# Kernel optimization log

Measured on AMD Instinct MI355X. Metric: run time of the kernel, lower is better.

The kernel has to match this reference:

```python
import jax, jax.numpy as jnp
import numpy as np

B, P, S, D, H, DFF, VOC = 8, 16, 512, 512, 8, 2048, 10000
DEPTH = D // H
SIGMA = 0.1
T = 256
LN_EPS = 1e-6


def setup_inputs() -> dict:
    key = jax.random.key(0)
    ks = jax.random.split(key, 40)
    n = lambda i, sh, sc=1.0: jax.random.normal(ks[i], sh, jnp.float32) * sc
    inp = {
        "r": n(0, (B, P, D)),
        "x": jax.random.randint(ks[1], (B, 1), 0, VOC),
        "K": n(2, (B, P, S, D)),
        "Vs": n(3, (B, P, S, D)),
        "w": jax.random.uniform(ks[4], (B, P, 1), jnp.float32),
        "I": jax.random.randint(ks[5], (B, P, S), 0, P),
        "t": T,
        "eps_q": n(6, (B, P, 1, D)),
        "eps_k": n(7, (B, P, 1, D)),
        "eps_v": n(8, (B, P, 1, D)),
        "eps_z": n(9, (B, P, 1, D)),
        "gumbel": -jnp.log(-jnp.log(jax.random.uniform(ks[10], (B, P, P), jnp.float32, 1e-8, 1.0))),
        "Wq": n(11, (D, D), 0.02), "bq": jnp.zeros((D,), jnp.float32),
        "Wk": n(12, (D, D), 0.02), "bk": jnp.zeros((D,), jnp.float32),
        "Wv": n(13, (D, D), 0.02), "bv": jnp.zeros((D,), jnp.float32),
        "Wo": n(14, (D, D), 0.02), "bo": jnp.zeros((D,), jnp.float32),
        "ln1_g": jnp.ones((D,), jnp.float32), "ln1_b": jnp.zeros((D,), jnp.float32),
        "ln3_g": jnp.ones((D,), jnp.float32), "ln3_b": jnp.zeros((D,), jnp.float32),
        "W1": n(15, (D, DFF), 0.02), "b1": jnp.zeros((DFF,), jnp.float32),
        "W2": n(16, (DFF, D), 0.02), "b2": jnp.zeros((D,), jnp.float32),
        "Wout": n(17, (D, VOC), 0.02), "bout": jnp.zeros((VOC,), jnp.float32),
    }
    return inp


def _layernorm(x, g, b):
    mu = jnp.mean(x, axis=-1, keepdims=True)
    var = jnp.mean((x - mu) ** 2, axis=-1, keepdims=True)
    return (x - mu) / jnp.sqrt(var + LN_EPS) * g + b


def _split_heads(x):  # (B,P,L,D) -> (B,P,H,L,depth)
    b, p, l, _ = x.shape
    return x.reshape(b, p, l, H, DEPTH).transpose(0, 1, 3, 2, 4)


def _resample(params, i_t, t):  # reorder particle axis on prefix [:t+1]
    pref = jnp.take_along_axis(params[:, :, :t + 1], i_t[:, :, None, None], axis=1)
    return jnp.concatenate([pref, params[:, :, t + 1:]], axis=2)


def reference(r, x, K, Vs, w, I, t, eps_q, eps_k, eps_v, eps_z, gumbel,
              Wq, bq, Wk, bk, Wv, bv, Wo, bo, ln1_g, ln1_b, ln3_g, ln3_b,
              W1, b1, W2, b2, Wout, bout):
    x = x.astype(jnp.int32)
    I = I.astype(jnp.int32)
    r4 = r[:, :, None, :]                                   # (B,P,1,D)
    # --- mha_smc: noisy projections + K/V buffer update at t ---
    q = r4 @ Wq + bq + SIGMA * eps_q
    k = r4 @ Wk + bk + SIGMA * eps_k
    v = r4 @ Wv + bv + SIGMA * eps_v
    K = K.at[:, :, t, :].set(k[:, :, 0, :])
    Vs = Vs.at[:, :, t, :].set(v[:, :, 0, :])
    qh = _split_heads(q)                                    # (B,P,H,1,depth)
    Kh = _split_heads(K)                                    # (B,P,H,S,depth)
    Vh = _split_heads(Vs)
    scores = jnp.einsum('bphqd,bphsd->bphqs', qh, Kh) / jnp.sqrt(jnp.float32(DEPTH))
    mask = (jnp.arange(S) <= t)[None, None, None, None, :]
    scores = jnp.where(mask, scores, jnp.float32(-1e9))
    attn = jax.nn.softmax(scores, axis=-1)                  # (B,P,H,1,S)
    zh = jnp.einsum('bphqs,bphsd->bphqd', attn, Vh)
    z = zh.transpose(0, 1, 3, 2, 4).reshape(B, P, 1, D) @ Wo + bo
    z = z + SIGMA * eps_z                                   # reparametrized output noise
    attn_weights = jnp.mean(attn, axis=2)                   # (B,P,1,S)
    # --- residual + FFN (dropout disabled: training=False) ---
    out1 = _layernorm(z + r4, ln1_g, ln1_b)
    ffn = jnp.maximum(out1 @ W1 + b1, 0.0) @ W2 + b2
    r_ = _layernorm(ffn + out1, ln3_g, ln3_b)
    predictions = r_ @ Wout + bout                          # (B,P,1,VOC)
    # --- classification importance weights ---
    probs = jax.nn.softmax(predictions, axis=-1)
    idx = jnp.broadcast_to(x.reshape(B, 1, 1, 1), (B, P, 1, 1))
    w_sq = jnp.take_along_axis(probs, idx, axis=-1)[:, :, 0, 0]  # (B,P)
    w_sq = jax.lax.stop_gradient(w_sq)
    pred2 = predictions[:, :, 0, :]                         # (B,P,VOC)
    w_for_pred = w_sq[:, :, None]
    good_avg_pred = jnp.mean(pred2, axis=1, keepdims=True)  # (B,1,VOC)
    avg_pred_after_softmax = jnp.mean(jax.nn.softmax(pred2, axis=-1), axis=1, keepdims=True)
    argmax_w = jnp.argmax(w_for_pred, axis=1)               # (B,1)
    max_prediction = jnp.take_along_axis(pred2, argmax_w[:, :, None], axis=1)  # (B,1,VOC)
    # --- sample_and_keep_indices: Gumbel-max categorical over particles ---
    logits = jnp.log(w_sq + 1e-10)                          # (B,P)
    i_t = jnp.argmax(logits[:, None, :] + gumbel, axis=-1).astype(jnp.int32)  # (B,P)
    I_pref = jnp.take_along_axis(I[:, :, :t], i_t[:, :, None], axis=1)
    I_new = jnp.concatenate([I_pref, i_t[:, :, None], I[:, :, t + 1:]], axis=2)
    # --- resampling (faithful to original: V resampled from already-resampled K) ---
    K = _resample(K, i_t, t)
    Vs = _resample(K, i_t, t)
    z = jnp.take_along_axis(z, I_new[:, :, t][:, :, None, None], axis=1)
    w_new = w_sq[:, :, None]
    return (r4, z, avg_pred_after_softmax, good_avg_pred, max_prediction,
            eps_z, attn_weights, K, Vs, w_new, I_new)
```

## Files before the change

### kernel.cpp

```cpp
#include <hip/hip_runtime.h>

#define NDFF 2048
#define NVOC 10000
#define SIGMA 0.1f

typedef float f32x4 __attribute__((ext_vector_type(4)));

#define O0 0
#define O1 65536
#define O2 131072
#define O3 211072
#define O4 291072
#define O5 371072
#define O6 436608
#define O7 502144
#define O8 34056576
#define O9 67611008
#define O10 67611136

#define WQ    0
#define WK    65536
#define WV    131072
#define WZH   196608
#define WZ    262144
#define WO1   327680
#define WH1   393216
#define WR    655360
#define WPRED 720896
#define WMAX  2000896
#define WSUM  2001024
#define WWSQ  2001152
#define WIT   2001280
#define WF2P  2001536
#define WSC   2263680

__global__ __launch_bounds__(512)
void k_qkv(const float* __restrict__ r,
           const float* __restrict__ Wq, const float* __restrict__ bq, const float* __restrict__ eq, float* __restrict__ oq,
           const float* __restrict__ Wk, const float* __restrict__ bk, const float* __restrict__ ek, float* __restrict__ ok,
           const float* __restrict__ Wv, const float* __restrict__ bv, const float* __restrict__ ev, float* __restrict__ ov)
{
    const float *W, *bias, *eps; float* out;
    if (blockIdx.z == 0)      { W = Wq; bias = bq; eps = eq; out = oq; }
    else if (blockIdx.z == 1) { W = Wk; bias = bk; eps = ek; out = ok; }
    else                      { W = Wv; bias = bv; eps = ev; out = ov; }
    int tid = threadIdx.x;
    int col = tid & 63, kq = tid >> 6;
    int colg = blockIdx.x * 64 + col;
    int row0 = blockIdx.y * 8;
    __shared__ float rs[8][512];
#pragma unroll
    for (int j = 0; j < 8; j++) {
        int idx = tid + j * 512;
        rs[idx >> 9][idx & 511] = r[(row0 + (idx >> 9)) * 512 + (idx & 511)];
    }
    __syncthreads();
    float acc[8] = {0,0,0,0,0,0,0,0};
    const float* Wp = W + (kq * 64) * 512 + colg;
#pragma unroll 8
    for (int d = 0; d < 64; d++) {
        float wv = Wp[d * 512];
#pragma unroll
        for (int p = 0; p < 8; p++) acc[p] += rs[p][kq * 64 + d] * wv;
    }
    __syncthreads();
    float (*part)[8][64] = (float(*)[8][64])rs;
#pragma unroll
    for (int p = 0; p < 8; p++) part[kq][p][col] = acc[p];
    __syncthreads();
    {
        int p = tid >> 6, c = tid & 63;
        int cg = blockIdx.x * 64 + c;
        float v = 0.f;
#pragma unroll
        for (int k = 0; k < 8; k++) v += part[k][p][c];
        out[(row0 + p) * 512 + cg] = v + bias[cg] + SIGMA * eps[(row0 + p) * 512 + cg];
    }
}

__global__ __launch_bounds__(256)
void k_attn(const float* __restrict__ qws, const float* __restrict__ kws,
            const float* __restrict__ vws, const float* __restrict__ Kin,
            const float* __restrict__ Vin, const int* __restrict__ t_ptr,
            float* __restrict__ zh, float* __restrict__ scw)
{
    int t = *t_ptr;
    int bp = blockIdx.x, h = blockIdx.y;
    int tid = threadIdx.x;
    int wave = tid >> 6, lane = tid & 63;
    __shared__ float sc[512];
    __shared__ float red[4], red2[4];
    __shared__ float part[4][64];

    float4 qv = ((const float4*)(qws + bp * 512 + h * 64))[lane & 15];

    for (int sb = wave * 4; sb <= t; sb += 16) {
        int s = sb + (lane >> 4);
        bool valid = (s <= t);
        int ss = valid ? s : t;
        const float4* kr = (ss == t) ? (const float4*)(kws + bp * 512 + h * 64)
                                     : (const float4*)(Kin + (bp * 512 + ss) * 512 + h * 64);
        float4 kv = kr[lane & 15];
        float p = qv.x * kv.x + qv.y * kv.y + qv.z * kv.z + qv.w * kv.w;
#pragma unroll
        for (int m = 1; m < 16; m <<= 1) p += __shfl_xor(p, m, 64);
        if ((lane & 15) == 0 && valid) sc[s] = p * 0.125f;
    }
    __syncthreads();

    float lm = -3.0e38f;
    for (int s = tid; s <= t; s += 256) lm = fmaxf(lm, sc[s]);
#pragma unroll
    for (int o = 32; o; o >>= 1) lm = fmaxf(lm, __shfl_xor(lm, o, 64));
    if (lane == 0) red[wave] = lm;
    __syncthreads();
    float m = fmaxf(fmaxf(red[0], red[1]), fmaxf(red[2], red[3]));
    float ls = 0.f;
    for (int s = tid; s <= t; s += 256) ls += __expf(sc[s] - m);
#pragma unroll
    for (int o = 32; o; o >>= 1) ls += __shfl_xor(ls, o, 64);
    if (lane == 0) red2[wave] = ls;
    __syncthreads();
    float inv = 1.f / (red2[0] + red2[1] + red2[2] + red2[3]);
    for (int s = tid; s <= t; s += 256) {
        float a = __expf(sc[s] - m) * inv;
        sc[s] = a;
        scw[(bp * 8 + h) * 512 + s] = a;
    }
    __syncthreads();

    float acc = 0.f;
    const float* Vp = Vin + (bp * 512) * 512 + h * 64 + lane;
    int s = wave;
    for (; s + 12 < t; s += 16) {
        float v0 = __builtin_nontemporal_load(Vp + (size_t)(s     ) * 512);
        float v1 = __builtin_nontemporal_load(Vp + (size_t)(s +  4) * 512);
        float v2 = __builtin_nontemporal_load(Vp + (size_t)(s +  8) * 512);
        float v3 = __builtin_nontemporal_load(Vp + (size_t)(s + 12) * 512);
        acc += sc[s] * v0 + sc[s + 4] * v1 + sc[s + 8] * v2 + sc[s + 12] * v3;
    }
    for (; s < t; s += 4) acc += sc[s] * __builtin_nontemporal_load(Vp + (size_t)s * 512);
    if ((t & 3) == wave) acc += sc[t] * vws[bp * 512 + h * 64 + lane];
    part[wave][lane] = acc;
    __syncthreads();
    if (tid < 64)
        zh[bp * 512 + h * 64 + tid] = part[0][tid] + part[1][tid] + part[2][tid] + part[3][tid];
}

__global__ __launch_bounds__(512)
void k_zproj(const float* __restrict__ zh, const float* __restrict__ Wo,
             const float* __restrict__ bo, const float* __restrict__ epsz,
             float* __restrict__ out)
{
    int tid = threadIdx.x;
    int col = tid & 63, kq = tid >> 6;
    int colg = blockIdx.x * 64 + col;
    int row0 = blockIdx.y * 8;
    __shared__ float rs[8][512];
#pragma unroll
    for (int j = 0; j < 8; j++) {
        int idx = tid + j * 512;
        rs[idx >> 9][idx & 511] = zh[(row0 + (idx >> 9)) * 512 + (idx & 511)];
    }
    __syncthreads();
    float acc[8] = {0,0,0,0,0,0,0,0};
    const float* Wp = Wo + (kq * 64) * 512 + colg;
#pragma unroll 8
    for (int d = 0; d < 64; d++) {
        float wv = Wp[d * 512];
#pragma unroll
        for (int p = 0; p < 8; p++) acc[p] += rs[p][kq * 64 + d] * wv;
    }
    __syncthreads();
    float (*part)[8][64] = (float(*)[8][64])rs;
#pragma unroll
    for (int p = 0; p < 8; p++) part[kq][p][col] = acc[p];
    __syncthreads();
    {
        int p = tid >> 6, c = tid & 63;
        int cg = blockIdx.x * 64 + c;
        float v = 0.f;
#pragma unroll
        for (int k = 0; k < 8; k++) v += part[k][p][c];
        out[(row0 + p) * 512 + cg] = v + bo[cg] + SIGMA * epsz[(row0 + p) * 512 + cg];
    }
}

__global__ __launch_bounds__(512)
void k_ln(const float* __restrict__ a, const float* __restrict__ b,
          const float* __restrict__ g, const float* __restrict__ beta,
          float* __restrict__ out)
{
    __shared__ float red[8];
    int row = blockIdx.x, tid = threadIdx.x;
    float x = a[row * 512 + tid] + b[row * 512 + tid];
    float s = x;
#pragma unroll
    for (int o = 32; o; o >>= 1) s += __shfl_xor(s, o, 64);
    if ((tid & 63) == 0) red[tid >> 6] = s;
    __syncthreads();
    float tot = 0.f;
#pragma unroll
    for (int i = 0; i < 8; i++) tot += red[i];
    float mu = tot * (1.f / 512.f);
    float dx = x - mu;
    float s2 = dx * dx;
#pragma unroll
    for (int o = 32; o; o >>= 1) s2 += __shfl_xor(s2, o, 64);
    __syncthreads();
    if ((tid & 63) == 0) red[tid >> 6] = s2;
    __syncthreads();
    float tot2 = 0.f;
#pragma unroll
    for (int i = 0; i < 8; i++) tot2 += red[i];
    float var = tot2 * (1.f / 512.f);
    out[row * 512 + tid] = dx * rsqrtf(var + 1e-6f) * g[tid] + beta[tid];
}

__global__ __launch_bounds__(512)
void k_ln_sum4(const float* __restrict__ f2p, const float* __restrict__ b2,
               const float* __restrict__ o1, const float* __restrict__ g,
               const float* __restrict__ beta, float* __restrict__ out)
{
    __shared__ float red[8];
    int row = blockIdx.x, tid = threadIdx.x;
    int idx = row * 512 + tid;
    float x = f2p[idx] + f2p[65536 + idx] + f2p[131072 + idx] + f2p[196608 + idx]
            + b2[tid] + o1[idx];
    float s = x;
#pragma unroll
    for (int o = 32; o; o >>= 1) s += __shfl_xor(s, o, 64);
    if ((tid & 63) == 0) red[tid >> 6] = s;
    __syncthreads();
    float tot = 0.f;
#pragma unroll
    for (int i = 0; i < 8; i++) tot += red[i];
    float mu = tot * (1.f / 512.f);
    float dx = x - mu;
    float s2 = dx * dx;
#pragma unroll
    for (int o = 32; o; o >>= 1) s2 += __shfl_xor(s2, o, 64);
    __syncthreads();
    if ((tid & 63) == 0) red[tid >> 6] = s2;
    __syncthreads();
    float tot2 = 0.f;
#pragma unroll
    for (int i = 0; i < 8; i++) tot2 += red[i];
    float var = tot2 * (1.f / 512.f);
    out[idx] = dx * rsqrtf(var + 1e-6f) * g[tid] + beta[tid];
}

__global__ __launch_bounds__(512)
void k_ffn1(const float* __restrict__ in, const float* __restrict__ W1,
            const float* __restrict__ b1, float* __restrict__ h1)
{
    int tid = threadIdx.x;
    int col = tid & 63, kq = tid >> 6;
    int colg = blockIdx.x * 64 + col;
    int row0 = blockIdx.y * 8;
    __shared__ float rs[8][512];
#pragma unroll
    for (int j = 0; j < 8; j++) {
        int idx = tid + j * 512;
        rs[idx >> 9][idx & 511] = in[(row0 + (idx >> 9)) * 512 + (idx & 511)];
    }
    __syncthreads();
    float acc[8] = {0,0,0,0,0,0,0,0};
    const float* Wp = W1 + (kq * 64) * NDFF + colg;
#pragma unroll 8
    for (int d = 0; d < 64; d++) {
        float wv = Wp[d * NDFF];
#pragma unroll
        for (int p = 0; p < 8; p++) acc[p] += rs[p][kq * 64 + d] * wv;
    }
    __syncthreads();
    float (*part)[8][64] = (float(*)[8][64])rs;
#pragma unroll
    for (int p = 0; p < 8; p++) part[kq][p][col] = acc[p];
    __syncthreads();
    {
        int p = tid >> 6, c = tid & 63;
        int cg = blockIdx.x * 64 + c;
        float v = 0.f;
#pragma unroll
        for (int k = 0; k < 8; k++) v += part[k][p][c];
        h1[(row0 + p) * NDFF + cg] = fmaxf(v + b1[cg], 0.f);
    }
}

__global__ __launch_bounds__(512)
void k_ffn2p(const float* __restrict__ h1, const float* __restrict__ W2,
             float* __restrict__ f2p)
{
    int tid = threadIdx.x;
    int col = tid & 63, kq = tid >> 6;
    int colg = blockIdx.x * 64 + col;
    int row0 = blockIdx.y * 8;
    int ks = blockIdx.z;
    __shared__ float rs[8][512];
#pragma unroll
    for (int j = 0; j < 8; j++) {
        int idx = tid + j * 512;
        rs[idx >> 9][idx & 511] = h1[(row0 + (idx >> 9)) * NDFF + ks * 512 + (idx & 511)];
    }
    __syncthreads();
    float acc[8] = {0,0,0,0,0,0,0,0};
    const float* Wp = W2 + (ks * 512 + kq * 64) * 512 + colg;
#pragma unroll 8
    for (int d = 0; d < 64; d++) {
        float wv = Wp[d * 512];
#pragma unroll
        for (int p = 0; p < 8; p++) acc[p] += rs[p][kq * 64 + d] * wv;
    }
    __syncthreads();
    float (*part)[8][64] = (float(*)[8][64])rs;
#pragma unroll
    for (int p = 0; p < 8; p++) part[kq][p][col] = acc[p];
    __syncthreads();
    {
        int p = tid >> 6, c = tid & 63;
        int cg = blockIdx.x * 64 + c;
        float v = 0.f;
#pragma unroll
        for (int k = 0; k < 8; k++) v += part[k][p][c];
        f2p[ks * 65536 + (row0 + p) * 512 + cg] = v;
    }
}

__global__ __launch_bounds__(512)
void k_pred(const float* __restrict__ r_, const float* __restrict__ Wout,
            const float* __restrict__ bout, float* __restrict__ pred)
{
    int tid = threadIdx.x;
    int col = tid & 255, kh = tid >> 8;
    int colg = blockIdx.x * 256 + col;
    int colL = min(colg, NVOC - 1);
    int row0 = blockIdx.y * 16;
    __shared__ float rs[16][512];
#pragma unroll
    for (int j = 0; j < 16; j++) {
        int idx = tid + j * 512;
        rs[idx >> 9][idx & 511] = r_[(row0 + (idx >> 9)) * 512 + (idx & 511)];
    }
    __syncthreads();
    float acc[16];
#pragma unroll
    for (int p = 0; p < 16; p++) acc[p] = 0.f;
    const float* Wp = Wout + (kh * 256) * NVOC + colL;
#pragma unroll 4
    for (int d = 0; d < 256; d++) {
        float wv = Wp[d * NVOC];
#pragma unroll
        for (int p = 0; p < 16; p++) acc[p] += rs[p][kh * 256 + d] * wv;
    }
    __syncthreads();
    float (*part)[256] = (float(*)[256])rs;
    if (kh == 1) {
#pragma unroll
        for (int p = 0; p < 16; p++) part[p][col] = acc[p];
    }
    __syncthreads();
    if (kh == 0 && colg < NVOC) {
        float bv = bout[colg];
#pragma unroll
        for (int p = 0; p < 16; p++)
            pred[(row0 + p) * NVOC + colg] = acc[p] + part[p][col] + bv;
    }
}

__global__ __launch_bounds__(512)
void k_soft(const float* __restrict__ pred, const int* __restrict__ x,
            const float* __restrict__ scw, const int* __restrict__ t_ptr,
            float* __restrict__ rowmax, float* __restrict__ rowsum,
            float* __restrict__ wsq, float* __restrict__ out)
{
    __shared__ float red[8];
    int row = blockIdx.x, tid = threadIdx.x;
    {
        int t = *t_ptr;
        float a = 0.f;
        if (tid <= t) {
#pragma unroll
            for (int hh = 0; hh < 8; hh++) a += scw[(row * 8 + hh) * 512 + tid];
            a *= 0.125f;
        }
        out[O6 + row * 512 + tid] = a;
    }
    const float* pr = pred + row * NVOC;
    float m = -3.0e38f;
    for (int v = tid; v < NVOC; v += 512) m = fmaxf(m, pr[v]);
#pragma unroll
    for (int o = 32; o; o >>= 1) m = fmaxf(m, __shfl_xor(m, o, 64));
    if ((tid & 63) == 0) red[tid >> 6] = m;
    __syncthreads();
#pragma unroll
    for (int i = 0; i < 8; i++) m = fmaxf(m, red[i]);
    __syncthreads();
    float s = 0.f;
    for (int v = tid; v < NVOC; v += 512) s += __expf(pr[v] - m);
#pragma unroll
    for (int o = 32; o; o >>= 1) s += __shfl_xor(s, o, 64);
    if ((tid & 63) == 0) red[tid >> 6] = s;
    __syncthreads();
    if (tid == 0) {
        float tot = 0.f;
#pragma unroll
        for (int i = 0; i < 8; i++) tot += red[i];
        rowmax[row] = m; rowsum[row] = tot;
        int b = row >> 4;
        float w = __expf(pr[x[b]] - m) / tot;
        wsq[row] = w;
        out[O9 + row] = w;
    }
}

__global__ __launch_bounds__(512)
void k_vocab(const float* __restrict__ pred, const float* __restrict__ rowmax,
             const float* __restrict__ rowsum, const float* __restrict__ wsq,
             const float* __restrict__ gumbel, int* __restrict__ it,
             float* __restrict__ out)
{
    int b = blockIdx.y;
    int tid = threadIdx.x;
    __shared__ int s_amw;
    if (tid == 0) {
        float bw = -3.0e38f; int bj = 0;
#pragma unroll
        for (int pp = 0; pp < 16; pp++) {
            float wv = wsq[b * 16 + pp];
            if (wv > bw) { bw = wv; bj = pp; }
        }
        s_amw = bj;
    }
    if (blockIdx.x == 0 && tid < 16) {
        float best = -3.0e38f; int bi = 0;
#pragma unroll
        for (int pp = 0; pp < 16; pp++) {
            float v = logf(wsq[b * 16 + pp] + 1e-10f) + gumbel[(b * 16 + tid) * 16 + pp];
            if (v > best) { best = v; bi = pp; }
        }
        it[b * 16 + tid] = bi;
    }
    __syncthreads();
    int v = blockIdx.x * 512 + tid;
    if (v >= NVOC) return;
    int amw = s_amw;
    float ga = 0.f, as = 0.f;
#pragma unroll
    for (int p = 0; p < 16; p++) {
        int rr = b * 16 + p;
        float pv = pred[rr * NVOC + v];
        ga += pv;
        as += __expf(pv - rowmax[rr]) * (1.f / rowsum[rr]);
    }
    out[O3 + b * NVOC + v] = ga * (1.f / 16.f);
    out[O2 + b * NVOC + v] = as * (1.f / 16.f);
    out[O4 + b * NVOC + v] = pred[(b * 16 + amw) * NVOC + v];
}

__global__ __launch_bounds__(256)
void k_resample(const float* __restrict__ Kin, const float* __restrict__ kws,
                const int* __restrict__ it, const int* __restrict__ t_ptr,
                const float* __restrict__ r, const float* __restrict__ epsz,
                const float* __restrict__ zws, const int* __restrict__ Iin,
                float* __restrict__ out)
{
    int t = *t_ptr;
    const f32x4* K4  = (const f32x4*)Kin;
    const f32x4* kw4 = (const f32x4*)kws;
    const f32x4* r4  = (const f32x4*)r;
    const f32x4* e4  = (const f32x4*)epsz;
    const f32x4* z4  = (const f32x4*)zws;
    f32x4* oK = (f32x4*)(out + O7);
    f32x4* oV = (f32x4*)(out + O8);
    const int total = 128 * 512 * 128;
    const int total2 = total + 16384;
    for (int i = blockIdx.x * 256 + threadIdx.x; i < total2; i += gridDim.x * 256) {
        if (i < total) {
            int lane = i & 127;
            int row = i >> 7;
            int s = row & 511;
            int bp = row >> 9;
            int b = bp >> 4;
            f32x4 vK, vV;
            if (s > t) {
                vK = __builtin_nontemporal_load(&K4[i]);
                vV = vK;
            } else {
                int ip = it[bp];
                int ip2 = it[b * 16 + ip];
                if (s == t) {
                    vK = kw4[(b * 16 + ip) * 128 + lane];
                    vV = kw4[(b * 16 + ip2) * 128 + lane];
                } else {
                    vK = K4[((b * 16 + ip) * 512 + s) * 128 + lane];
                    vV = K4[((b * 16 + ip2) * 512 + s) * 128 + lane];
                }
            }
            __builtin_nontemporal_store(vK, &oK[i]);
            __builtin_nontemporal_store(vV, &oV[i]);
        } else {
            int j = i - total;
            int fidx = j * 4;
            ((f32x4*)(out + O0))[j] = r4[j];
            ((f32x4*)(out + O5))[j] = e4[j];
            int row = fidx >> 9, d0 = fidx & 511;
            int b = row >> 4;
            int ip = it[row];
            ((f32x4*)(out + O1))[j] = z4[((b * 16 + ip) << 7) + (d0 >> 2)];
#pragma unroll
            for (int k = 0; k < 4; k++) {
                int s = d0 + k;
                float iv;
                if (s < t)       iv = (float)Iin[((b * 16 + ip) << 9) + s];
                else if (s == t) iv = (float)ip;
                else             iv = (float)Iin[row * 512 + s];
                out[O10 + fidx + k] = iv;
            }
        }
    }
}

extern "C" void kernel_launch(void* const* d_in, const int* in_sizes, int n_in,
                              void* d_out, int out_size, void* d_ws, size_t ws_size,
                              hipStream_t stream) {
    const float* r      = (const float*)d_in[0];
    const int*   x      = (const int*)d_in[1];
    const float* Kin    = (const float*)d_in[2];
    const float* Vin    = (const float*)d_in[3];
    const int*   Iin    = (const int*)d_in[5];
    const int*   t_ptr  = (const int*)d_in[6];
    const float* eps_q  = (const float*)d_in[7];
    const float* eps_k  = (const float*)d_in[8];
    const float* eps_v  = (const float*)d_in[9];
    const float* eps_z  = (const float*)d_in[10];
    const float* gumbel = (const float*)d_in[11];
    const float* Wq = (const float*)d_in[12]; const float* bq = (const float*)d_in[13];
    const float* Wk = (const float*)d_in[14]; const float* bk = (const float*)d_in[15];
    const float* Wv = (const float*)d_in[16]; const float* bv = (const float*)d_in[17];
    const float* Wo = (const float*)d_in[18]; const float* bo = (const float*)d_in[19];
    const float* ln1_g = (const float*)d_in[20]; const float* ln1_b = (const float*)d_in[21];
    const float* ln3_g = (const float*)d_in[22]; const float* ln3_b = (const float*)d_in[23];
    const float* W1 = (const float*)d_in[24]; const float* b1 = (const float*)d_in[25];
    const float* W2 = (const float*)d_in[26]; const float* b2 = (const float*)d_in[27];
    const float* Wout = (const float*)d_in[28]; const float* bout = (const float*)d_in[29];

    float* ws  = (float*)d_ws;
    float* q   = ws + WQ;
    float* kv  = ws + WK;
    float* vv  = ws + WV;
    float* zh  = ws + WZH;
    float* zp  = ws + WZ;
    float* o1  = ws + WO1;
    float* h1  = ws + WH1;
    float* rr  = ws + WR;
    float* pr  = ws + WPRED;
    float* rmx = ws + WMAX;
    float* rsm = ws + WSUM;
    float* wsq = ws + WWSQ;
    int*   itw = (int*)(ws + WIT);
    float* f2p = ws + WF2P;
    float* scw = ws + WSC;
    float* outp = (float*)d_out;

    k_qkv<<<dim3(8, 16, 3), 512, 0, stream>>>(r, Wq, bq, eps_q, q, Wk, bk, eps_k, kv, Wv, bv, eps_v, vv);
    k_attn<<<dim3(128, 8), 256, 0, stream>>>(q, kv, vv, Kin, Vin, t_ptr, zh, scw);
    k_zproj<<<dim3(8, 16), 512, 0, stream>>>(zh, Wo, bo, eps_z, zp);
    k_ln<<<128, 512, 0, stream>>>(zp, r, ln1_g, ln1_b, o1);
    k_ffn1<<<dim3(32, 16), 512, 0, stream>>>(o1, W1, b1, h1);
    k_ffn2p<<<dim3(8, 16, 4), 512, 0, stream>>>(h1, W2, f2p);
    k_ln_sum4<<<128, 512, 0, stream>>>(f2p, b2, o1, ln3_g, ln3_b, rr);
    k_pred<<<dim3(40, 8), 512, 0, stream>>>(rr, Wout, bout, pr);
    k_soft<<<128, 512, 0, stream>>>(pr, x, scw, t_ptr, rmx, rsm, wsq, outp);
    k_vocab<<<dim3(20, 8), 512, 0, stream>>>(pr, rmx, rsm, wsq, gumbel, itw, outp);
    k_resample<<<4096, 256, 0, stream>>>(Kin, kv, itw, t_ptr, r, eps_z, zp, Iin, outp);
}
```

Before: 199.8 us.

## Fuse layernorms into FFN1 and prediction GEMMs, widen attention blocks

The two standalone layernorm kernels are removed. LN1 is recomputed inside each k_ffn1 block, with the x==0 blocks writing o1. LN3, together with the four-way f2p split-K sum, moves into k_pred's shared-memory prologue. This drops two launches and the intermediate round trip through global memory, at the cost of redundant layernorm work in every column block. Attention blocks also grow from 256 to 512 threads so each block streams more V rows in parallel.

```diff
diff --git a/kernel.cpp b/kernel.cpp
--- a/kernel.cpp
+++ b/kernel.cpp
@@ -25,7 +25,6 @@
 #define WZ    262144
 #define WO1   327680
 #define WH1   393216
-#define WR    655360
 #define WPRED 720896
 #define WMAX  2000896
 #define WSUM  2001024
@@ -50,10 +49,7 @@
     int row0 = blockIdx.y * 8;
     __shared__ float rs[8][512];
 #pragma unroll
-    for (int j = 0; j < 8; j++) {
-        int idx = tid + j * 512;
-        rs[idx >> 9][idx & 511] = r[(row0 + (idx >> 9)) * 512 + (idx & 511)];
-    }
+    for (int j = 0; j < 8; j++) rs[j][tid & 511] = r[(row0 + j) * 512 + tid];
     __syncthreads();
     float acc[8] = {0,0,0,0,0,0,0,0};
     const float* Wp = W + (kq * 64) * 512 + colg;
@@ -78,7 +74,7 @@
     }
 }
 
-__global__ __launch_bounds__(256)
+__global__ __launch_bounds__(512)
 void k_attn(const float* __restrict__ qws, const float* __restrict__ kws,
             const float* __restrict__ vws, const float* __restrict__ Kin,
             const float* __restrict__ Vin, const int* __restrict__ t_ptr,
@@ -89,12 +85,12 @@
     int tid = threadIdx.x;
     int wave = tid >> 6, lane = tid & 63;
     __shared__ float sc[512];
-    __shared__ float red[4], red2[4];
-    __shared__ float part[4][64];
+    __shared__ float red[8], red2[8];
+    __shared__ float part[8][64];
 
     float4 qv = ((const float4*)(qws + bp * 512 + h * 64))[lane & 15];
 
-    for (int sb = wave * 4; sb <= t; sb += 16) {
+    for (int sb = wave * 4; sb <= t; sb += 32) {
         int s = sb + (lane >> 4);
         bool valid = (s <= t);
         int ss = valid ? s : t;
@@ -109,20 +105,25 @@
     __syncthreads();
 
     float lm = -3.0e38f;
-    for (int s = tid; s <= t; s += 256) lm = fmaxf(lm, sc[s]);
+    for (int s = tid; s <= t; s += 512) lm = fmaxf(lm, sc[s]);
 #pragma unroll
     for (int o = 32; o; o >>= 1) lm = fmaxf(lm, __shfl_xor(lm, o, 64));
     if (lane == 0) red[wave] = lm;
     __syncthreads();
-    float m = fmaxf(fmaxf(red[0], red[1]), fmaxf(red[2], red[3]));
+    float m = red[0];
+#pragma unroll
+    for (int i = 1; i < 8; i++) m = fmaxf(m, red[i]);
     float ls = 0.f;
-    for (int s = tid; s <= t; s += 256) ls += __expf(sc[s] - m);
+    for (int s = tid; s <= t; s += 512) ls += __expf(sc[s] - m);
 #pragma unroll
     for (int o = 32; o; o >>= 1) ls += __shfl_xor(ls, o, 64);
     if (lane == 0) red2[wave] = ls;
     __syncthreads();
-    float inv = 1.f / (red2[0] + red2[1] + red2[2] + red2[3]);
-    for (int s = tid; s <= t; s += 256) {
+    float tot = 0.f;
+#pragma unroll
+    for (int i = 0; i < 8; i++) tot += red2[i];
+    float inv = 1.f / tot;
+    for (int s = tid; s <= t; s += 512) {
         float a = __expf(sc[s] - m) * inv;
         sc[s] = a;
         scw[(bp * 8 + h) * 512 + s] = a;
@@ -132,19 +133,23 @@
     float acc = 0.f;
     const float* Vp = Vin + (bp * 512) * 512 + h * 64 + lane;
     int s = wave;
-    for (; s + 12 < t; s += 16) {
+    for (; s + 24 < t; s += 32) {
         float v0 = __builtin_nontemporal_load(Vp + (size_t)(s     ) * 512);
-        float v1 = __builtin_nontemporal_load(Vp + (size_t)(s +  4) * 512);
-        float v2 = __builtin_nontemporal_load(Vp + (size_t)(s +  8) * 512);
-        float v3 = __builtin_nontemporal_load(Vp + (size_t)(s + 12) * 512);
-        acc += sc[s] * v0 + sc[s + 4] * v1 + sc[s + 8] * v2 + sc[s + 12] * v3;
-    }
-    for (; s < t; s += 4) acc += sc[s] * __builtin_nontemporal_load(Vp + (size_t)s * 512);
-    if ((t & 3) == wave) acc += sc[t] * vws[bp * 512 + h * 64 + lane];
+        float v1 = __builtin_nontemporal_load(Vp + (size_t)(s +  8) * 512);
+        float v2 = __builtin_nontemporal_load(Vp + (size_t)(s + 16) * 512);
+        float v3 = __builtin_nontemporal_load(Vp + (size_t)(s + 24) * 512);
+        acc += sc[s] * v0 + sc[s + 8] * v1 + sc[s + 16] * v2 + sc[s + 24] * v3;
+    }
+    for (; s < t; s += 8) acc += sc[s] * __builtin_nontemporal_load(Vp + (size_t)s * 512);
+    if ((t & 7) == wave) acc += sc[t] * vws[bp * 512 + h * 64 + lane];
     part[wave][lane] = acc;
     __syncthreads();
-    if (tid < 64)
-        zh[bp * 512 + h * 64 + tid] = part[0][tid] + part[1][tid] + part[2][tid] + part[3][tid];
+    if (tid < 64) {
+        float v = 0.f;
+#pragma unroll
+        for (int k = 0; k < 8; k++) v += part[k][tid];
+        zh[bp * 512 + h * 64 + tid] = v;
+    }
 }
 
 __global__ __launch_bounds__(512)
@@ -158,10 +163,7 @@
     int row0 = blockIdx.y * 8;
     __shared__ float rs[8][512];
 #pragma unroll
-    for (int j = 0; j < 8; j++) {
-        int idx = tid + j * 512;
-        rs[idx >> 9][idx & 511] = zh[(row0 + (idx >> 9)) * 512 + (idx & 511)];
-    }
+    for (int j = 0; j < 8; j++) rs[j][tid] = zh[(row0 + j) * 512 + tid];
     __syncthreads();
     float acc[8] = {0,0,0,0,0,0,0,0};
     const float* Wp = Wo + (kq * 64) * 512 + colg;
@@ -187,82 +189,42 @@
 }
 
 __global__ __launch_bounds__(512)
-void k_ln(const float* __restrict__ a, const float* __restrict__ b,
-          const float* __restrict__ g, const float* __restrict__ beta,
-          float* __restrict__ out)
-{
-    __shared__ float red[8];
-    int row = blockIdx.x, tid = threadIdx.x;
-    float x = a[row * 512 + tid] + b[row * 512 + tid];
-    float s = x;
-#pragma unroll
-    for (int o = 32; o; o >>= 1) s += __shfl_xor(s, o, 64);
-    if ((tid & 63) == 0) red[tid >> 6] = s;
-    __syncthreads();
-    float tot = 0.f;
-#pragma unroll
-    for (int i = 0; i < 8; i++) tot += red[i];
-    float mu = tot * (1.f / 512.f);
-    float dx = x - mu;
-    float s2 = dx * dx;
-#pragma unroll
-    for (int o = 32; o; o >>= 1) s2 += __shfl_xor(s2, o, 64);
-    __syncthreads();
-    if ((tid & 63) == 0) red[tid >> 6] = s2;
-    __syncthreads();
-    float tot2 = 0.f;
-#pragma unroll
-    for (int i = 0; i < 8; i++) tot2 += red[i];
-    float var = tot2 * (1.f / 512.f);
-    out[row * 512 + tid] = dx * rsqrtf(var + 1e-6f) * g[tid] + beta[tid];
-}
-
-__global__ __launch_bounds__(512)
-void k_ln_sum4(const float* __restrict__ f2p, const float* __restrict__ b2,
-               const float* __restrict__ o1, const float* __restrict__ g,
-               const float* __restrict__ beta, float* __restrict__ out)
-{
-    __shared__ float red[8];
-    int row = blockIdx.x, tid = threadIdx.x;
-    int idx = row * 512 + tid;
-    float x = f2p[idx] + f2p[65536 + idx] + f2p[131072 + idx] + f2p[196608 + idx]
-            + b2[tid] + o1[idx];
-    float s = x;
-#pragma unroll
-    for (int o = 32; o; o >>= 1) s += __shfl_xor(s, o, 64);
-    if ((tid & 63) == 0) red[tid >> 6] = s;
-    __syncthreads();
-    float tot = 0.f;
-#pragma unroll
-    for (int i = 0; i < 8; i++) tot += red[i];
-    float mu = tot * (1.f / 512.f);
-    float dx = x - mu;
-    float s2 = dx * dx;
-#pragma unroll
-    for (int o = 32; o; o >>= 1) s2 += __shfl_xor(s2, o, 64);
-    __syncthreads();
-    if ((tid & 63) == 0) red[tid >> 6] = s2;
-    __syncthreads();
-    float tot2 = 0.f;
-#pragma unroll
-    for (int i = 0; i < 8; i++) tot2 += red[i];
-    float var = tot2 * (1.f / 512.f);
-    out[idx] = dx * rsqrtf(var + 1e-6f) * g[tid] + beta[tid];
-}
-
-__global__ __launch_bounds__(512)
-void k_ffn1(const float* __restrict__ in, const float* __restrict__ W1,
-            const float* __restrict__ b1, float* __restrict__ h1)
+void k_ffn1(const float* __restrict__ zp, const float* __restrict__ r,
+            const float* __restrict__ g, const float* __restrict__ be,
+            const float* __restrict__ W1, const float* __restrict__ b1,
+            float* __restrict__ o1, float* __restrict__ h1)
 {
     int tid = threadIdx.x;
     int col = tid & 63, kq = tid >> 6;
     int colg = blockIdx.x * 64 + col;
     int row0 = blockIdx.y * 8;
     __shared__ float rs[8][512];
+    __shared__ float sm[8], si[8];
+    int wave = tid >> 6, lane = tid & 63;
 #pragma unroll
     for (int j = 0; j < 8; j++) {
-        int idx = tid + j * 512;
-        rs[idx >> 9][idx & 511] = in[(row0 + (idx >> 9)) * 512 + (idx & 511)];
+        int gi = (row0 + j) * 512 + tid;
+        rs[j][tid] = zp[gi] + r[gi];
+    }
+    __syncthreads();
+    {
+        float s = 0.f;
+        for (int c = lane; c < 512; c += 64) s += rs[wave][c];
+#pragma unroll
+        for (int o = 32; o; o >>= 1) s += __shfl_xor(s, o, 64);
+        float mu = s * (1.f / 512.f);
+        float v = 0.f;
+        for (int c = lane; c < 512; c += 64) { float dx = rs[wave][c] - mu; v += dx * dx; }
+#pragma unroll
+        for (int o = 32; o; o >>= 1) v += __shfl_xor(v, o, 64);
+        if (lane == 0) { sm[wave] = mu; si[wave] = rsqrtf(v * (1.f / 512.f) + 1e-6f); }
+    }
+    __syncthreads();
+#pragma unroll
+    for (int j = 0; j < 8; j++) {
+        float val = (rs[j][tid] - sm[j]) * si[j] * g[tid] + be[tid];
+        rs[j][tid] = val;
+        if (blockIdx.x == 0) o1[(row0 + j) * 512 + tid] = val;
     }
     __syncthreads();
     float acc[8] = {0,0,0,0,0,0,0,0};
@@ -299,10 +261,8 @@
     int ks = blockIdx.z;
     __shared__ float rs[8][512];
 #pragma unroll
-    for (int j = 0; j < 8; j++) {
-        int idx = tid + j * 512;
-        rs[idx >> 9][idx & 511] = h1[(row0 + (idx >> 9)) * NDFF + ks * 512 + (idx & 511)];
-    }
+    for (int j = 0; j < 8; j++)
+        rs[j][tid] = h1[(row0 + j) * NDFF + ks * 512 + tid];
     __syncthreads();
     float acc[8] = {0,0,0,0,0,0,0,0};
     const float* Wp = W2 + (ks * 512 + kq * 64) * 512 + colg;
@@ -328,7 +288,9 @@
 }
 
 __global__ __launch_bounds__(512)
-void k_pred(const float* __restrict__ r_, const float* __restrict__ Wout,
+void k_pred(const float* __restrict__ f2p, const float* __restrict__ b2,
+            const float* __restrict__ o1, const float* __restrict__ g3,
+            const float* __restrict__ b3, const float* __restrict__ Wout,
             const float* __restrict__ bout, float* __restrict__ pred)
 {
     int tid = threadIdx.x;
@@ -337,11 +299,33 @@
     int colL = min(colg, NVOC - 1);
     int row0 = blockIdx.y * 16;
     __shared__ float rs[16][512];
+    __shared__ float sm[16], si[16];
+    int wave = tid >> 6, lane = tid & 63;
 #pragma unroll
     for (int j = 0; j < 16; j++) {
-        int idx = tid + j * 512;
-        rs[idx >> 9][idx & 511] = r_[(row0 + (idx >> 9)) * 512 + (idx & 511)];
-    }
+        int gi = (row0 + j) * 512 + tid;
+        rs[j][tid] = f2p[gi] + f2p[65536 + gi] + f2p[131072 + gi] + f2p[196608 + gi]
+                   + b2[tid] + o1[gi];
+    }
+    __syncthreads();
+    {
+        int row = wave * 2 + (lane >> 5);
+        int l = lane & 31;
+        float s = 0.f;
+        for (int c = l; c < 512; c += 32) s += rs[row][c];
+#pragma unroll
+        for (int o = 16; o; o >>= 1) s += __shfl_xor(s, o, 64);
+        float mu = s * (1.f / 512.f);
+        float v = 0.f;
+        for (int c = l; c < 512; c += 32) { float dx = rs[row][c] - mu; v += dx * dx; }
+#pragma unroll
+        for (int o = 16; o; o >>= 1) v += __shfl_xor(v, o, 64);
+        if (l == 0) { sm[row] = mu; si[row] = rsqrtf(v * (1.f / 512.f) + 1e-6f); }
+    }
+    __syncthreads();
+#pragma unroll
+    for (int j = 0; j < 16; j++)
+        rs[j][tid] = (rs[j][tid] - sm[j]) * si[j] * g3[tid] + b3[tid];
     __syncthreads();
     float acc[16];
 #pragma unroll
@@ -553,7 +537,6 @@
     float* zp  = ws + WZ;
     float* o1  = ws + WO1;
     float* h1  = ws + WH1;
-    float* rr  = ws + WR;
     float* pr  = ws + WPRED;
     float* rmx = ws + WMAX;
     float* rsm = ws + WSUM;
@@ -564,13 +547,11 @@
     float* outp = (float*)d_out;
 
     k_qkv<<<dim3(8, 16, 3), 512, 0, stream>>>(r, Wq, bq, eps_q, q, Wk, bk, eps_k, kv, Wv, bv, eps_v, vv);
-    k_attn<<<dim3(128, 8), 256, 0, stream>>>(q, kv, vv, Kin, Vin, t_ptr, zh, scw);
+    k_attn<<<dim3(128, 8), 512, 0, stream>>>(q, kv, vv, Kin, Vin, t_ptr, zh, scw);
     k_zproj<<<dim3(8, 16), 512, 0, stream>>>(zh, Wo, bo, eps_z, zp);
-    k_ln<<<128, 512, 0, stream>>>(zp, r, ln1_g, ln1_b, o1);
-    k_ffn1<<<dim3(32, 16), 512, 0, stream>>>(o1, W1, b1, h1);
+    k_ffn1<<<dim3(32, 16), 512, 0, stream>>>(zp, r, ln1_g, ln1_b, W1, b1, o1, h1);
     k_ffn2p<<<dim3(8, 16, 4), 512, 0, stream>>>(h1, W2, f2p);
-    k_ln_sum4<<<128, 512, 0, stream>>>(f2p, b2, o1, ln3_g, ln3_b, rr);
-    k_pred<<<dim3(40, 8), 512, 0, stream>>>(rr, Wout, bout, pr);
+    k_pred<<<dim3(40, 8), 512, 0, stream>>>(f2p, b2, o1, ln3_g, ln3_b, Wout, bout, pr);
     k_soft<<<128, 512, 0, stream>>>(pr, x, scw, t_ptr, rmx, rsm, wsq, outp);
     k_vocab<<<dim3(20, 8), 512, 0, stream>>>(pr, rmx, rsm, wsq, gumbel, itw, outp);
     k_resample<<<4096, 256, 0, stream>>>(Kin, kv, itw, t_ptr, r, eps_z, zp, Iin, outp);
```

Measured after the change: 199.5 us, median of 2. About the same (-0.2%).
